# Performance work log

Hardware: AMD Instinct MI355X
Metric: run time of the kernel (lower is better)

Reference implementation:

```python
import jax, jax.numpy as jnp
import numpy as np

N, PAIR, M, D, O, R = 4096, 2, 64, 128, 128, 2
MAX_DEG = 32


def setup_inputs() -> dict:
    key = jax.random.key(0)
    k1, k2, k3, k4, k5, k6 = jax.random.split(key, 6)
    node_features = jax.random.normal(k1, (N, PAIR, M, D), dtype=jnp.float32)
    deg = jax.random.randint(k2, (N,), 0, MAX_DEG, dtype=jnp.int32)
    # per-relation Linear params (stored as [in, out]) and self-loop Linear
    W_r = jax.random.normal(k3, (R, D, O), dtype=jnp.float32) / np.sqrt(D)
    b_r = jax.random.normal(k4, (R, O), dtype=jnp.float32) * 0.01
    W0 = jax.random.normal(k5, (D, O), dtype=jnp.float32) / np.sqrt(D)
    b0 = jax.random.normal(k6, (O,), dtype=jnp.float32) * 0.01
    return {"node_features": node_features, "deg": deg, "W_r": W_r,
            "b_r": b_r, "W0": W0, "b0": b0}


def reference(node_features, deg, W_r, b_r, W0, b0):
    # Original: for each relation r, for each neighbor, adds W_r(x_i);
    # i.e. sum_r deg_i * (x_i @ W_r + b_r) = deg_i * (x_i @ sum_r W_r + sum_r b_r)
    Wsum = W_r.sum(axis=0)          # [D, O]
    bsum = b_r.sum(axis=0)          # [O]
    rel = jnp.einsum('npmd,do->npmo', node_features, Wsum) + bsum
    self_term = jnp.einsum('npmd,do->npmo', node_features, W0) + b0
    d = deg.astype(node_features.dtype)[:, None, None, None]
    h = jax.nn.relu(d * rel + self_term)  # [N, 2, M, O]
    # edge representation: mm(h_i, h_j.T) per entity -> [N, M, M]
    out = jnp.einsum('nmo,nko->nmk', h[:, 0], h[:, 1])
    return out
```

## Files before the change

### kernel.cpp

```cpp
#include <hip/hip_runtime.h>
#include <hip/hip_bf16.h>


typedef __attribute__((ext_vector_type(8))) short bf16x8;
typedef __attribute__((ext_vector_type(4))) float f32x4;

__device__ __forceinline__ unsigned int pkbf(float a, float b) {
    union { __hip_bfloat162 h; unsigned int u; } v;
    v.h = __float22bfloat162_rn(float2{a, b});
    return v.u;
}

__global__ __launch_bounds__(256) void build_weights(
    const float* __restrict__ W_r,
    const float* __restrict__ b_r,
    const float* __restrict__ W0,
    const float* __restrict__ b0,
    unsigned short* __restrict__ wfrag,
    float* __restrict__ call)
{
    int t = blockIdx.x * blockDim.x + threadIdx.x;
    int lane = t & 63;
    int ks = (t >> 6) & 3;
    int ct = (t >> 8) & 7;
    int d  = (t >> 11) & 31;
    int o = ct * 16 + (lane & 15);
    int kbase = ks * 32 + (lane >> 4) * 8;
    unsigned int* dst = (unsigned int*)(wfrag + (size_t)t * 8);
#pragma unroll
    for (int j = 0; j < 4; ++j) {
        int k0 = kbase + 2 * j;
        float wA = (float)d * (W_r[k0 * 128 + o] + W_r[128 * 128 + k0 * 128 + o]) + W0[k0 * 128 + o];
        float wB = (float)d * (W_r[(k0 + 1) * 128 + o] + W_r[128 * 128 + (k0 + 1) * 128 + o]) + W0[(k0 + 1) * 128 + o];
        dst[j] = pkbf(wA, wB);
    }
    if (t < 32 * 128) {
        int dd = t >> 7, oo = t & 127;
        call[t] = (float)dd * (b_r[oo] + b_r[128 + oo]) + b0[oo];
    }
}

__global__ __launch_bounds__(256) void edge_kernel(
    const float* __restrict__ x,
    const int* __restrict__ deg,
    const unsigned short* __restrict__ wfrag,
    const float* __restrict__ call,
    float* __restrict__ out)
{
    __shared__ unsigned short hlds[128 * 128];

    const int n = blockIdx.x;
    const int tid = threadIdx.x;
    const int wave = tid >> 6;
    const int lane = tid & 63;
    const int l15 = lane & 15;
    const int lhi = lane >> 4;
    const int d = deg[n];

    const float* xn = x + (size_t)n * (2 * 64 * 128);
    const unsigned short* wf = wfrag + (size_t)d * (8 * 4 * 64 * 8);
    const float* cd = call + d * 128;

    const int rbase = wave * 32;
    bf16x8 afrag[2][4];
#pragma unroll
    for (int rt = 0; rt < 2; ++rt) {
        const float* rowp = xn + (size_t)(rbase + rt * 16 + l15) * 128;
#pragma unroll
        for (int ks = 0; ks < 4; ++ks) {
            const f32x4* p = (const f32x4*)(rowp + ks * 32 + lhi * 8);
            f32x4 a0 = p[0];
            f32x4 a1 = p[1];
            union { bf16x8 v; unsigned int u[4]; } f;
            f.u[0] = pkbf(a0.x, a0.y);
            f.u[1] = pkbf(a0.z, a0.w);
            f.u[2] = pkbf(a1.x, a1.y);
            f.u[3] = pkbf(a1.z, a1.w);
            afrag[rt][ks] = f.v;
        }
    }

#pragma unroll
    for (int ct = 0; ct < 8; ++ct) {
        bf16x8 bfrag[4];
#pragma unroll
        for (int ks = 0; ks < 4; ++ks)
            bfrag[ks] = *(const bf16x8*)(wf + ((size_t)(ct * 4 + ks) * 64 + lane) * 8);
        const f32x4 cc4 = *(const f32x4*)(cd + ct * 16 + lhi * 4);
#pragma unroll
        for (int rt = 0; rt < 2; ++rt) {
            f32x4 acc = {0.f, 0.f, 0.f, 0.f};
#pragma unroll
            for (int ks = 0; ks < 4; ++ks)
                acc = __builtin_amdgcn_mfma_f32_16x16x32_bf16(bfrag[ks], afrag[rt][ks], acc, 0, 0, 0);
            float h0v = fmaxf(acc[0] + cc4.x, 0.f);
            float h1v = fmaxf(acc[1] + cc4.y, 0.f);
            float h2v = fmaxf(acc[2] + cc4.z, 0.f);
            float h3v = fmaxf(acc[3] + cc4.w, 0.f);
            union { unsigned int u[2]; unsigned long long ull; } pk;
            pk.u[0] = pkbf(h0v, h1v);
            pk.u[1] = pkbf(h2v, h3v);
            int m = rbase + rt * 16 + l15;
            int chunk = (ct * 2 + (lhi >> 1)) ^ (m & 7);
            int byteoff = m * 256 + chunk * 16 + (lhi & 1) * 8;
            *(unsigned long long*)((char*)hlds + byteoff) = pk.ull;
        }
    }
    __syncthreads();

    const int mrow = wave * 16 + l15;
    bf16x8 hb[4];
#pragma unroll
    for (int ks = 0; ks < 4; ++ks) {
        int chunk = (ks * 4 + lhi) ^ (mrow & 7);
        hb[ks] = *(const bf16x8*)((const char*)hlds + mrow * 256 + chunk * 16);
    }
    float* outn = out + (size_t)n * 4096;
#pragma unroll
    for (int qt = 0; qt < 4; ++qt) {
        int qrow = 64 + qt * 16 + l15;
        f32x4 acc = {0.f, 0.f, 0.f, 0.f};
#pragma unroll
        for (int ks = 0; ks < 4; ++ks) {
            int chunk = (ks * 4 + lhi) ^ (qrow & 7);
            bf16x8 ha = *(const bf16x8*)((const char*)hlds + qrow * 256 + chunk * 16);
            acc = __builtin_amdgcn_mfma_f32_16x16x32_bf16(ha, hb[ks], acc, 0, 0, 0);
        }
        *(f32x4*)(outn + mrow * 64 + qt * 16 + lhi * 4) = acc;
    }
}

extern "C" void kernel_launch(void* const* d_in, const int* in_sizes, int n_in,
                              void* d_out, int out_size, void* d_ws, size_t ws_size,
                              hipStream_t stream) {
    const float* x   = (const float*)d_in[0];
    const int*   deg = (const int*)d_in[1];
    const float* W_r = (const float*)d_in[2];
    const float* b_r = (const float*)d_in[3];
    const float* W0  = (const float*)d_in[4];
    const float* b0  = (const float*)d_in[5];
    float* out = (float*)d_out;

    unsigned short* wfrag = (unsigned short*)d_ws;
    float* call = (float*)((unsigned short*)d_ws + 32 * 8 * 4 * 64 * 8);

    build_weights<<<256, 256, 0, stream>>>(W_r, b_r, W0, b0, wfrag, call);
    edge_kernel<<<4096, 256, 0, stream>>>(x, deg, wfrag, call, out);
}
```

Before: 81.36 us.

## Stage weight fragments cooperatively in LDS and reuse the buffer for h

Each block now loads the 32 KB degree-specific weight-fragment slice once, cooperatively, into shared memory. Previously every wave fetched all of it from global/L2 on its own. The raw x loads are issued alongside this staging before the bf16 conversion. The projection loop processes two column tiles at a time with interleaved MFMAs and synchronises before overwriting each consumed weight region with h. The h storage changes to a per-column-tile layout with a new swizzle. The trade-off is four times fewer global weight reads for extra barriers and more register pressure.

```diff
diff --git a/kernel.cpp b/kernel.cpp
--- a/kernel.cpp
+++ b/kernel.cpp
@@ -47,7 +47,8 @@
     const float* __restrict__ call,
     float* __restrict__ out)
 {
-    __shared__ unsigned short hlds[128 * 128];
+    __shared__ unsigned short hlds[16384];
+    char* const ldsb = (char*)hlds;
 
     const int n = blockIdx.x;
     const int tid = threadIdx.x;
@@ -58,19 +59,38 @@
     const int d = deg[n];
 
     const float* xn = x + (size_t)n * (2 * 64 * 128);
-    const unsigned short* wf = wfrag + (size_t)d * (8 * 4 * 64 * 8);
+    const char* wsrc = (const char*)(wfrag + (size_t)d * (8 * 4 * 64 * 8));
     const float* cd = call + d * 128;
+
+    f32x4 wst[8];
+#pragma unroll
+    for (int i = 0; i < 8; ++i)
+        wst[i] = *(const f32x4*)(wsrc + i * 4096 + tid * 16);
 
     const int rbase = wave * 32;
     bf16x8 afrag[2][4];
+    f32x4 xraw[2][4][2];
 #pragma unroll
     for (int rt = 0; rt < 2; ++rt) {
         const float* rowp = xn + (size_t)(rbase + rt * 16 + l15) * 128;
 #pragma unroll
         for (int ks = 0; ks < 4; ++ks) {
             const f32x4* p = (const f32x4*)(rowp + ks * 32 + lhi * 8);
-            f32x4 a0 = p[0];
-            f32x4 a1 = p[1];
+            xraw[rt][ks][0] = p[0];
+            xraw[rt][ks][1] = p[1];
+        }
+    }
+
+#pragma unroll
+    for (int i = 0; i < 8; ++i)
+        *(f32x4*)(ldsb + i * 4096 + tid * 16) = wst[i];
+
+#pragma unroll
+    for (int rt = 0; rt < 2; ++rt)
+#pragma unroll
+        for (int ks = 0; ks < 4; ++ks) {
+            f32x4 a0 = xraw[rt][ks][0];
+            f32x4 a1 = xraw[rt][ks][1];
             union { bf16x8 v; unsigned int u[4]; } f;
             f.u[0] = pkbf(a0.x, a0.y);
             f.u[1] = pkbf(a0.z, a0.w);
@@ -78,33 +98,63 @@
             f.u[3] = pkbf(a1.z, a1.w);
             afrag[rt][ks] = f.v;
         }
-    }
-
-#pragma unroll
-    for (int ct = 0; ct < 8; ++ct) {
-        bf16x8 bfrag[4];
-#pragma unroll
-        for (int ks = 0; ks < 4; ++ks)
-            bfrag[ks] = *(const bf16x8*)(wf + ((size_t)(ct * 4 + ks) * 64 + lane) * 8);
-        const f32x4 cc4 = *(const f32x4*)(cd + ct * 16 + lhi * 4);
+
+    __syncthreads();
+
+    f32x4 ccA = *(const f32x4*)(cd + 0 * 16 + lhi * 4);
+    f32x4 ccB = *(const f32x4*)(cd + 1 * 16 + lhi * 4);
+#pragma unroll
+    for (int p = 0; p < 4; ++p) {
+        const int ct0 = 2 * p, ct1 = 2 * p + 1;
+        bf16x8 bf0[4], bf1[4];
+#pragma unroll
+        for (int ks = 0; ks < 4; ++ks) {
+            bf0[ks] = *(const bf16x8*)(ldsb + ct0 * 4096 + ks * 1024 + lane * 16);
+            bf1[ks] = *(const bf16x8*)(ldsb + ct1 * 4096 + ks * 1024 + lane * 16);
+        }
+        f32x4 acc0[2] = {{0.f,0.f,0.f,0.f},{0.f,0.f,0.f,0.f}};
+        f32x4 acc1[2] = {{0.f,0.f,0.f,0.f},{0.f,0.f,0.f,0.f}};
+#pragma unroll
+        for (int ks = 0; ks < 4; ++ks) {
+#pragma unroll
+            for (int rt = 0; rt < 2; ++rt) {
+                acc0[rt] = __builtin_amdgcn_mfma_f32_16x16x32_bf16(bf0[ks], afrag[rt][ks], acc0[rt], 0, 0, 0);
+                acc1[rt] = __builtin_amdgcn_mfma_f32_16x16x32_bf16(bf1[ks], afrag[rt][ks], acc1[rt], 0, 0, 0);
+            }
+        }
+        const int ctn = (p < 3) ? (2 * p + 2) : 0;
+        f32x4 ccA_n = *(const f32x4*)(cd + ctn * 16 + lhi * 4);
+        f32x4 ccB_n = *(const f32x4*)(cd + (ctn + 1) * 16 + lhi * 4);
+
+        __syncthreads();
+
 #pragma unroll
         for (int rt = 0; rt < 2; ++rt) {
-            f32x4 acc = {0.f, 0.f, 0.f, 0.f};
-#pragma unroll
-            for (int ks = 0; ks < 4; ++ks)
-                acc = __builtin_amdgcn_mfma_f32_16x16x32_bf16(bfrag[ks], afrag[rt][ks], acc, 0, 0, 0);
-            float h0v = fmaxf(acc[0] + cc4.x, 0.f);
-            float h1v = fmaxf(acc[1] + cc4.y, 0.f);
-            float h2v = fmaxf(acc[2] + cc4.z, 0.f);
-            float h3v = fmaxf(acc[3] + cc4.w, 0.f);
-            union { unsigned int u[2]; unsigned long long ull; } pk;
-            pk.u[0] = pkbf(h0v, h1v);
-            pk.u[1] = pkbf(h2v, h3v);
-            int m = rbase + rt * 16 + l15;
-            int chunk = (ct * 2 + (lhi >> 1)) ^ (m & 7);
-            int byteoff = m * 256 + chunk * 16 + (lhi & 1) * 8;
-            *(unsigned long long*)((char*)hlds + byteoff) = pk.ull;
-        }
+            const int m = rbase + rt * 16 + l15;
+            const int slot = ((lhi >> 1) ^ ((m >> 2) & 1));
+            {
+                float h0v = fmaxf(acc0[rt][0] + ccA.x, 0.f);
+                float h1v = fmaxf(acc0[rt][1] + ccA.y, 0.f);
+                float h2v = fmaxf(acc0[rt][2] + ccA.z, 0.f);
+                float h3v = fmaxf(acc0[rt][3] + ccA.w, 0.f);
+                union { unsigned int u[2]; unsigned long long ull; } pk;
+                pk.u[0] = pkbf(h0v, h1v);
+                pk.u[1] = pkbf(h2v, h3v);
+                *(unsigned long long*)(ldsb + ct0 * 4096 + m * 32 + slot * 16 + (lhi & 1) * 8) = pk.ull;
+            }
+            {
+                float h0v = fmaxf(acc1[rt][0] + ccB.x, 0.f);
+                float h1v = fmaxf(acc1[rt][1] + ccB.y, 0.f);
+                float h2v = fmaxf(acc1[rt][2] + ccB.z, 0.f);
+                float h3v = fmaxf(acc1[rt][3] + ccB.w, 0.f);
+                union { unsigned int u[2]; unsigned long long ull; } pk;
+                pk.u[0] = pkbf(h0v, h1v);
+                pk.u[1] = pkbf(h2v, h3v);
+                *(unsigned long long*)(ldsb + ct1 * 4096 + m * 32 + slot * 16 + (lhi & 1) * 8) = pk.ull;
+            }
+        }
+        ccA = ccA_n;
+        ccB = ccB_n;
     }
     __syncthreads();
 
@@ -112,18 +162,20 @@
     bf16x8 hb[4];
 #pragma unroll
     for (int ks = 0; ks < 4; ++ks) {
-        int chunk = (ks * 4 + lhi) ^ (mrow & 7);
-        hb[ks] = *(const bf16x8*)((const char*)hlds + mrow * 256 + chunk * 16);
+        const int ct = ks * 2 + (lhi >> 1);
+        const int s  = (lhi & 1) ^ ((mrow >> 2) & 1);
+        hb[ks] = *(const bf16x8*)(ldsb + ct * 4096 + mrow * 32 + s * 16);
     }
     float* outn = out + (size_t)n * 4096;
 #pragma unroll
     for (int qt = 0; qt < 4; ++qt) {
-        int qrow = 64 + qt * 16 + l15;
+        const int qrow = 64 + qt * 16 + l15;
         f32x4 acc = {0.f, 0.f, 0.f, 0.f};
 #pragma unroll
         for (int ks = 0; ks < 4; ++ks) {
-            int chunk = (ks * 4 + lhi) ^ (qrow & 7);
-            bf16x8 ha = *(const bf16x8*)((const char*)hlds + qrow * 256 + chunk * 16);
+            const int ct = ks * 2 + (lhi >> 1);
+            const int s  = (lhi & 1) ^ ((qrow >> 2) & 1);
+            bf16x8 ha = *(const bf16x8*)(ldsb + ct * 4096 + qrow * 32 + s * 16);
             acc = __builtin_amdgcn_mfma_f32_16x16x32_bf16(ha, hb[ks], acc, 0, 0, 0);
         }
         *(f32x4*)(outn + mrow * 64 + qt * 16 + lhi * 4) = acc;
```

After: 76.49 us. -6.0%, faster.
